# Optimization experiments

Measured on AMD Instinct MI355X. Metric: run time of the kernel, lower is better.

## Reference

```python
import jax, jax.numpy as jnp
import numpy as np

# Dimensions
B, T_ENC, T_DEC = 64, 128, 64          # batch, encoder frames, max_video_length
DH, DV, CHUNK = 1024, 2048, 8          # dim_hidden, dim_video, ON-LSTM chunk size
NCH = DV // CHUNK                      # number of chunks (256)
G = 4 * DV + 2 * NCH                   # gate width of ON-LSTM cell


def setup_inputs() -> dict:
    key = jax.random.key(0)
    ks = jax.random.split(key, 6)
    s = lambda n: 1.0 / np.sqrt(n)
    return {
        "encoder_outputs": jax.random.normal(ks[0], (B, T_ENC, DH), jnp.float32),
        "encoder_hidden": jnp.zeros((1, B, DH), jnp.float32),  # unused by forward
        # Attention_update params: score over concat(enc_feat, query)
        "W_att1": (jax.random.normal(ks[1], (DH + DV, DH), jnp.float32) * s(DH + DV)),
        "b_att1": jnp.zeros((DH,), jnp.float32),
        "w_att2": (jax.random.normal(ks[2], (DH,), jnp.float32) * s(DH)),
        # ON-LSTM cell params (single layer: input DH -> hidden DV)
        "W_ih": (jax.random.normal(ks[3], (DH, G), jnp.float32) * s(DH)),
        "b_ih": jnp.zeros((G,), jnp.float32),
        "W_hh": (jax.random.normal(ks[4], (DV, G), jnp.float32) * s(DV)),
        "b_hh": jnp.zeros((G,), jnp.float32),
    }


def cumsoftmax(x):
    return jnp.cumsum(jax.nn.softmax(x, axis=-1), axis=-1)


def _decode(encoder_outputs, W_att1, b_att1, w_att2, W_ih, b_ih, W_hh, b_hh):
    b = encoder_outputs.shape[0]
    t_enc = encoder_outputs.shape[1]
    h0 = jnp.zeros((b, DV), encoder_outputs.dtype)
    c0 = jnp.zeros((b, NCH, CHUNK), encoder_outputs.dtype)

    def step(carry, _):
        h, c = carry
        # --- attention: additive score over encoder outputs, query = hidden ---
        q = jnp.broadcast_to(h[:, None, :], (b, t_enc, DV))
        feat = jnp.concatenate([encoder_outputs, q], axis=-1)        # (B,T,DH+DV)
        e = jnp.tanh(feat @ W_att1 + b_att1) @ w_att2                # (B,T)
        alpha = jax.nn.softmax(e, axis=-1)
        context = jnp.einsum("bt,btd->bd", alpha, encoder_outputs)  # (B,DH)
        # --- ON-LSTM cell ---
        gates = context @ W_ih + b_ih + h @ W_hh + b_hh              # (B,G)
        cingate = 1.0 - cumsoftmax(gates[:, :NCH])                   # master input gate
        cforgetgate = cumsoftmax(gates[:, NCH:2 * NCH])              # master forget gate
        r = gates[:, 2 * NCH:].reshape(b, 4 * NCH, CHUNK)
        o = jax.nn.sigmoid(r[:, :NCH])
        g = jnp.tanh(r[:, NCH:2 * NCH])
        i = jax.nn.sigmoid(r[:, 2 * NCH:3 * NCH])
        f = jax.nn.sigmoid(r[:, 3 * NCH:])
        cin = cingate[:, :, None]
        cfg = cforgetgate[:, :, None]
        overlap = cfg * cin
        fgate = f * overlap + (cfg - overlap)
        igate = i * overlap + (cin - overlap)
        cy = fgate * c + igate * g                                   # (B,NCH,CHUNK)
        hy = (o * jnp.tanh(cy)).reshape(b, DV)
        return (hy, cy), hy

    (_, _), outs = jax.lax.scan(step, (h0, c0), None, length=T_DEC)
    return jnp.transpose(outs, (1, 0, 2))  # (B, T_DEC, DV)


def reference(encoder_outputs, encoder_hidden, W_att1, b_att1, w_att2, W_ih, b_ih, W_hh, b_hh):
    return _decode(encoder_outputs, W_att1, b_att1, w_att2, W_ih, b_ih, W_hh, b_hh)
```

## Files before the change

### kernel.cpp

```cpp
#include <hip/hip_runtime.h>
#include <math.h>

#define BB   64
#define TENC 128
#define TDEC 64
#define DHH  1024
#define DVV  2048
#define NCHN 256
#define GG   8704
#define KTOT 3072

typedef unsigned short u16;
typedef __bf16 bf16x8 __attribute__((ext_vector_type(8)));
typedef float  f32x4  __attribute__((ext_vector_type(4)));

__device__ __forceinline__ u16 f2bf(float f) {
    unsigned u = __float_as_uint(f);
    unsigned r = (u + 0x7fffu + ((u >> 16) & 1u)) >> 16;
    return (u16)r;
}
__device__ __forceinline__ float bf2f(u16 s) { return __uint_as_float(((unsigned)s) << 16); }
__device__ __forceinline__ float tanh_fast(float x) {
    float xc = fminf(fmaxf(x, -15.f), 15.f);
    float t = __expf(2.f * xc);
    return 1.f - 2.f * __builtin_amdgcn_rcpf(t + 1.f);
}
__device__ __forceinline__ float sigmoid_fast(float x) {
    float xc = fminf(fmaxf(x, -30.f), 30.f);
    return __builtin_amdgcn_rcpf(1.f + __expf(-xc));
}


__global__ __launch_bounds__(256) void k_init2(float* __restrict__ c,
                                               u16* __restrict__ xh,
                                               u16* __restrict__ xl) {
    int i = blockIdx.x * 256 + threadIdx.x;
    xh[i] = 0; xl[i] = 0;
    if (i < BB * DVV) c[i] = 0.f;
}

template <bool LO>
__global__ __launch_bounds__(256) void k_cvt(const float* __restrict__ S1,
                                             const float* __restrict__ S2,
                                             int K1, int N, int K,
                                             u16* __restrict__ Dh,
                                             u16* __restrict__ Dl) {
    __shared__ float t[64][65];
    int n0 = blockIdx.x * 64, k0 = blockIdx.y * 64;
    int tid = threadIdx.x;
    int cn = tid & 63, r4 = tid >> 6;
#pragma unroll
    for (int p = 0; p < 16; ++p) {
        int kk = p * 4 + r4;
        int kg = k0 + kk;
        const float* src = (kg < K1) ? S1 + (size_t)kg * N : S2 + (size_t)(kg - K1) * N;
        t[kk][cn] = src[n0 + cn];
    }
    __syncthreads();
    int ck = tid & 63, n4 = tid >> 6;
#pragma unroll
    for (int p = 0; p < 16; ++p) {
        int nn = p * 4 + n4;
        float w = t[ck][nn];
        u16 hi = f2bf(w);
        size_t o = (size_t)(n0 + nn) * K + k0 + ck;
        Dh[o] = hi;
        if (LO) Dl[o] = f2bf(w - bf2f(hi));
    }
}

__global__ __launch_bounds__(256) void k_cvt_rm(const float* __restrict__ src,
                                                u16* __restrict__ dh,
                                                u16* __restrict__ dl, int n) {
    for (int i = blockIdx.x * 256 + threadIdx.x; i < n; i += gridDim.x * 256) {
        float w = src[i];
        u16 hi = f2bf(w);
        dh[i] = hi;
        dl[i] = f2bf(w - bf2f(hi));
    }
}

__global__ __launch_bounds__(256) void k_mmaP(const u16* __restrict__ ench,
                                              const u16* __restrict__ encl,
                                              const u16* __restrict__ W1h,
                                              const u16* __restrict__ W1l,
                                              const float* __restrict__ b1,
                                              float* __restrict__ P) {
    int n0 = blockIdx.x * 64, m0 = blockIdx.y * 64;
    int wv = threadIdx.x >> 6, l = threadIdx.x & 63;
    int lr = l & 15, lk = (l >> 4) * 8;
    int n = n0 + wv * 16 + lr;
    const u16* wph = W1h + (size_t)n * DHH + lk;
    const u16* wpl = W1l + (size_t)n * DHH + lk;
    const u16* aph = ench + (size_t)(m0 + lr) * DHH + lk;
    const u16* apl = encl + (size_t)(m0 + lr) * DHH + lk;
    f32x4 z = {0.f, 0.f, 0.f, 0.f};
    f32x4 acc[4] = {z, z, z, z};
    for (int k = 0; k < DHH; k += 32) {
        bf16x8 bh = *(const bf16x8*)(wph + k);
        bf16x8 bl = *(const bf16x8*)(wpl + k);
#pragma unroll
        for (int mf = 0; mf < 4; ++mf) {
            size_t ao = (size_t)mf * 16 * DHH + k;
            bf16x8 ah = *(const bf16x8*)(aph + ao);
            bf16x8 al = *(const bf16x8*)(apl + ao);
            acc[mf] = __builtin_amdgcn_mfma_f32_16x16x32_bf16(ah, bh, acc[mf], 0, 0, 0);
            acc[mf] = __builtin_amdgcn_mfma_f32_16x16x32_bf16(ah, bl, acc[mf], 0, 0, 0);
            acc[mf] = __builtin_amdgcn_mfma_f32_16x16x32_bf16(al, bh, acc[mf], 0, 0, 0);
        }
    }
    float bias = b1[n];
#pragma unroll
    for (int mf = 0; mf < 4; ++mf)
#pragma unroll
        for (int r = 0; r < 4; ++r) {
            int m = m0 + mf * 16 + (l >> 4) * 4 + r;
            P[(size_t)m * DHH + n] = acc[mf][r] + bias;
        }
}

__global__ __launch_bounds__(256) void k_P(const float* __restrict__ enc,
                                           const float* __restrict__ W1,
                                           const float* __restrict__ b1,
                                           float* __restrict__ P) {
    __shared__ float As[32][68];
    __shared__ float Bs[32][68];
    int j0 = blockIdx.x * 64;
    int m0 = blockIdx.y * 64;
    int tid = threadIdx.x;
    int jg = tid & 15, bg = tid >> 4;
    float acc[4][4] = {};
    for (int k0 = 0; k0 < DHH; k0 += 32) {
#pragma unroll
        for (int p = 0; p < 8; ++p) {
            int r = p * 8 + (tid >> 5);
            int kk = tid & 31;
            As[kk][r] = enc[(size_t)(m0 + r) * DHH + k0 + kk];
        }
#pragma unroll
        for (int p = 0; p < 8; ++p) {
            int kk = p * 4 + (tid >> 6);
            int jl = tid & 63;
            Bs[kk][jl] = W1[(size_t)(k0 + kk) * DHH + j0 + jl];
        }
        __syncthreads();
#pragma unroll
        for (int kk = 0; kk < 32; ++kk) {
            float4 a = *(const float4*)&As[kk][bg * 4];
            float4 b = *(const float4*)&Bs[kk][jg * 4];
            float av[4] = {a.x, a.y, a.z, a.w};
            float bv[4] = {b.x, b.y, b.z, b.w};
#pragma unroll
            for (int i = 0; i < 4; ++i)
#pragma unroll
                for (int j = 0; j < 4; ++j) acc[i][j] += av[i] * bv[j];
        }
        __syncthreads();
    }
    float4 bb = *(const float4*)&b1[j0 + jg * 4];
    float bia[4] = {bb.x, bb.y, bb.z, bb.w};
#pragma unroll
    for (int i = 0; i < 4; ++i) {
        int r = m0 + bg * 4 + i;
        float4 v = make_float4(acc[i][0] + bia[0], acc[i][1] + bia[1],
                               acc[i][2] + bia[2], acc[i][3] + bia[3]);
        *(float4*)&P[(size_t)r * DHH + j0 + jg * 4] = v;
    }
}


__global__ __launch_bounds__(512) void k_mma1(const u16* __restrict__ xh,
                                              const u16* __restrict__ Wta,
                                              float* __restrict__ hWp) {
    __shared__ float red[64 * 68];
    int n0 = blockIdx.x * 64;
    int kseg = blockIdx.y;
    int tid = threadIdx.x;
    int wv = tid >> 6, l = tid & 63;
    int wn = wv & 3, kh = wv >> 2;
    int lr = l & 15, lk = (l >> 4) * 8;
    int n = n0 + wn * 16 + lr;
    const u16* wp = Wta + (size_t)n * 2048 + lk;
    const u16* ap = xh + (size_t)lr * KTOT + 1024 + lk;
    f32x4 z = {0.f, 0.f, 0.f, 0.f};
    f32x4 acc[4] = {z, z, z, z};
    int kbeg = kseg * 256 + kh * 128;
    for (int k = kbeg; k < kbeg + 128; k += 32) {
        bf16x8 bfrag = *(const bf16x8*)(wp + k);
#pragma unroll
        for (int mf = 0; mf < 4; ++mf) {
            bf16x8 a = *(const bf16x8*)(ap + (size_t)mf * 16 * KTOT + k);
            acc[mf] = __builtin_amdgcn_mfma_f32_16x16x32_bf16(a, bfrag, acc[mf], 0, 0, 0);
        }
    }
    int moff = (l >> 4) * 4;
    if (kh == 0) {
#pragma unroll
        for (int mf = 0; mf < 4; ++mf)
#pragma unroll
            for (int r = 0; r < 4; ++r)
                red[(mf * 16 + moff + r) * 68 + wn * 16 + lr] = acc[mf][r];
    }
    __syncthreads();
    if (kh == 1) {
        float* dst = hWp + (size_t)kseg * 64 * DHH;
#pragma unroll
        for (int mf = 0; mf < 4; ++mf)
#pragma unroll
            for (int r = 0; r < 4; ++r) {
                int m = mf * 16 + moff + r;
                dst[(size_t)m * DHH + n] = acc[mf][r] + red[m * 68 + wn * 16 + lr];
            }
    }
}

template <int SEG>
__global__ __launch_bounds__(512) void k_mma3(const u16* __restrict__ xh,
                                              const u16* __restrict__ xl,
                                              const u16* __restrict__ Wh,
                                              const u16* __restrict__ Wl,
                                              float* __restrict__ part) {
    __shared__ float red[64 * 68];
    int n0 = blockIdx.x * 64;
    int kseg = blockIdx.y;
    int tid = threadIdx.x;
    int wv = tid >> 6, l = tid & 63;
    int wn = wv & 3, kh = wv >> 2;
    int lr = l & 15, lk = (l >> 4) * 8;
    int n = n0 + wn * 16 + lr;
    const u16* wph = Wh + (size_t)n * KTOT + lk;
    const u16* wpl = Wl + (size_t)n * KTOT + lk;
    const u16* aph = xh + (size_t)lr * KTOT + lk;
    const u16* apl = xl + (size_t)lr * KTOT + lk;
    f32x4 z = {0.f, 0.f, 0.f, 0.f};
    f32x4 acc[4] = {z, z, z, z};
    const int KSEG = KTOT / SEG;
    const int KH = KSEG / 2;
    int kbeg = kseg * KSEG + kh * KH;
    for (int k = kbeg; k < kbeg + KH; k += 32) {
        bf16x8 bh = *(const bf16x8*)(wph + k);
        bf16x8 bl = *(const bf16x8*)(wpl + k);
#pragma unroll
        for (int mf = 0; mf < 4; ++mf) {
            size_t ao = (size_t)mf * 16 * KTOT + k;
            bf16x8 ah = *(const bf16x8*)(aph + ao);
            bf16x8 al = *(const bf16x8*)(apl + ao);
            acc[mf] = __builtin_amdgcn_mfma_f32_16x16x32_bf16(ah, bh, acc[mf], 0, 0, 0);
            acc[mf] = __builtin_amdgcn_mfma_f32_16x16x32_bf16(ah, bl, acc[mf], 0, 0, 0);
            acc[mf] = __builtin_amdgcn_mfma_f32_16x16x32_bf16(al, bh, acc[mf], 0, 0, 0);
        }
    }
    int moff = (l >> 4) * 4;
    if (kh == 0) {
#pragma unroll
        for (int mf = 0; mf < 4; ++mf)
#pragma unroll
            for (int r = 0; r < 4; ++r)
                red[(mf * 16 + moff + r) * 68 + wn * 16 + lr] = acc[mf][r];
    }
    __syncthreads();
    if (kh == 1) {
        float* dst = part + (size_t)kseg * 64 * GG;
#pragma unroll
        for (int mf = 0; mf < 4; ++mf)
#pragma unroll
            for (int r = 0; r < 4; ++r) {
                int m = mf * 16 + moff + r;
                dst[(size_t)m * GG + n] = acc[mf][r] + red[m * 68 + wn * 16 + lr];
            }
    }
}

__global__ __launch_bounds__(256) void k_e(const float* __restrict__ P,
                                           const float* __restrict__ hWp,
                                           const float* __restrict__ w2,
                                           float* __restrict__ e) {
    int b = blockIdx.x, tg = blockIdx.y;
    __shared__ float hw[DHH];
    __shared__ float w2s[DHH];
    int tid = threadIdx.x;
    {
        float4 s = {0.f, 0.f, 0.f, 0.f};
#pragma unroll
        for (int ks = 0; ks < 8; ++ks) {
            float4 v = *(const float4*)&hWp[(size_t)(ks * 64 + b) * DHH + tid * 4];
            s.x += v.x; s.y += v.y; s.z += v.z; s.w += v.w;
        }
        *(float4*)&hw[tid * 4] = s;
        *(float4*)&w2s[tid * 4] = *(const float4*)&w2[tid * 4];
    }
    __syncthreads();
    int wave = tid >> 6, lane = tid & 63;
    const float* Pb = P + (size_t)b * TENC * DHH;
    for (int tt = 0; tt < 8; ++tt) {
        int t = tg * 32 + wave * 8 + tt;
        const float* Pr = Pb + (size_t)t * DHH;
        float s = 0.f;
#pragma unroll
        for (int i = 0; i < 16; ++i) {
            int d = i * 64 + lane;
            s += tanh_fast(Pr[d] + hw[d]) * w2s[d];
        }
#pragma unroll
        for (int off = 32; off > 0; off >>= 1) s += __shfl_down(s, off);
        if (lane == 0) e[b * TENC + t] = s;
    }
}

__global__ __launch_bounds__(256) void k_sc2(const float* __restrict__ e,
                                             const float* __restrict__ enc,
                                             u16* __restrict__ xh,
                                             u16* __restrict__ xl) {
    int b = blockIdx.x, dq = blockIdx.y;
    __shared__ float al[TENC];
    __shared__ float red[256];
    __shared__ float4 pr[4][64];
    int tid = threadIdx.x;
    float v = (tid < TENC) ? e[b * TENC + tid] : -3.0e38f;
    red[tid] = v;
    __syncthreads();
    for (int s = 128; s > 0; s >>= 1) {
        if (tid < s) red[tid] = fmaxf(red[tid], red[tid + s]);
        __syncthreads();
    }
    float mx = red[0];
    __syncthreads();
    float ex = (tid < TENC) ? __expf(v - mx) : 0.f;
    red[tid] = ex;
    __syncthreads();
    for (int s = 128; s > 0; s >>= 1) {
        if (tid < s) red[tid] += red[tid + s];
        __syncthreads();
    }
    float inv = 1.f / red[0];
    if (tid < TENC) al[tid] = ex * inv;
    __syncthreads();
    int w = tid >> 6, l = tid & 63;
    int dbase = dq * 256 + l * 4;
    const float* ep = enc + ((size_t)b * TENC + w * 32) * DHH + dbase;
    float4 acc = {0.f, 0.f, 0.f, 0.f};
#pragma unroll 8
    for (int tt = 0; tt < 32; ++tt) {
        float a = al[w * 32 + tt];
        float4 vv = *(const float4*)(ep + (size_t)tt * DHH);
        acc.x += a * vv.x; acc.y += a * vv.y; acc.z += a * vv.z; acc.w += a * vv.w;
    }
    pr[w][l] = acc;
    __syncthreads();
    if (tid < 64) {
        float4 a0 = pr[0][tid], a1 = pr[1][tid], a2 = pr[2][tid], a3 = pr[3][tid];
        float r0 = a0.x + a1.x + a2.x + a3.x;
        float r1 = a0.y + a1.y + a2.y + a3.y;
        float r2 = a0.z + a1.z + a2.z + a3.z;
        float r3 = a0.w + a1.w + a2.w + a3.w;
        size_t o = (size_t)b * KTOT + dq * 256 + tid * 4;
        u16 h0 = f2bf(r0), h1 = f2bf(r1), h2 = f2bf(r2), h3 = f2bf(r3);
        ushort4 hv = {h0, h1, h2, h3};
        ushort4 lv = {f2bf(r0 - bf2f(h0)), f2bf(r1 - bf2f(h1)),
                      f2bf(r2 - bf2f(h2)), f2bf(r3 - bf2f(h3))};
        *(ushort4*)&xh[o] = hv;
        *(ushort4*)&xl[o] = lv;
    }
}

__global__ __launch_bounds__(256) void k_pw2(const float* __restrict__ part, int nseg,
                                             const float* __restrict__ bih,
                                             const float* __restrict__ bhh,
                                             u16* __restrict__ xh,
                                             u16* __restrict__ xl,
                                             float* __restrict__ c,
                                             float* __restrict__ out, int t) {
    int b = blockIdx.x;
    __shared__ float g[GG];
    __shared__ float cs1[NCHN], cs2[NCHN], t1[NCHN], t2[NCHN];
    int tid = threadIdx.x;
    for (int p = 0; p < 34; ++p) {
        int j = p * 256 + tid;
        float s = bih[j] + bhh[j];
        for (int ks = 0; ks < nseg; ++ks) s += part[(size_t)(ks * 64 + b) * GG + j];
        g[j] = s;
    }
    __syncthreads();
    float x1 = g[tid], x2 = g[NCHN + tid];
    t1[tid] = x1; t2[tid] = x2;
    __syncthreads();
    for (int s = 128; s > 0; s >>= 1) {
        if (tid < s) { t1[tid] = fmaxf(t1[tid], t1[tid + s]); t2[tid] = fmaxf(t2[tid], t2[tid + s]); }
        __syncthreads();
    }
    float m1 = t1[0], m2 = t2[0];
    __syncthreads();
    float e1 = __expf(x1 - m1), e2 = __expf(x2 - m2);
    t1[tid] = e1; t2[tid] = e2;
    __syncthreads();
    for (int s = 128; s > 0; s >>= 1) {
        if (tid < s) { t1[tid] += t1[tid + s]; t2[tid] += t2[tid + s]; }
        __syncthreads();
    }
    float inv1 = 1.f / t1[0], inv2 = 1.f / t2[0];
    __syncthreads();
    cs1[tid] = e1; cs2[tid] = e2;
    __syncthreads();
    for (int off = 1; off < NCHN; off <<= 1) {
        float a1 = (tid >= off) ? cs1[tid - off] : 0.f;
        float a2 = (tid >= off) ? cs2[tid - off] : 0.f;
        __syncthreads();
        cs1[tid] += a1; cs2[tid] += a2;
        __syncthreads();
    }
    float* cb = c + (size_t)b * DVV;
    float* ob = out + ((size_t)b * TDEC + t) * DVV;
    u16* xhb = xh + (size_t)b * KTOT + 1024;
    u16* xlb = xl + (size_t)b * KTOT + 1024;
    for (int p = 0; p < 8; ++p) {
        int idx = p * 256 + tid;
        int ch = idx >> 3;
        float cin = 1.f - cs1[ch] * inv1;
        float cfg = cs2[ch] * inv2;
        float ov = cfg * cin;
        float oo = sigmoid_fast(g[512 + idx]);
        float gg = tanh_fast(g[2560 + idx]);
        float ii = sigmoid_fast(g[4608 + idx]);
        float ff = sigmoid_fast(g[6656 + idx]);
        float fg = ff * ov + (cfg - ov);
        float ig = ii * ov + (cin - ov);
        float cy = fg * cb[idx] + ig * gg;
        cb[idx] = cy;
        float hy = oo * tanh_fast(cy);
        ob[idx] = hy;
        u16 hh = f2bf(hy);
        xhb[idx] = hh;
        xlb[idx] = f2bf(hy - bf2f(hh));
    }
}


extern "C" void kernel_launch(void* const* d_in, const int* in_sizes, int n_in,
                              void* d_out, int out_size, void* d_ws, size_t ws_size,
                              hipStream_t stream) {
    const float* enc    = (const float*)d_in[0];
    const float* W_att1 = (const float*)d_in[2];
    const float* b_att1 = (const float*)d_in[3];
    const float* w_att2 = (const float*)d_in[4];
    const float* W_ih   = (const float*)d_in[5];
    const float* b_ih   = (const float*)d_in[6];
    const float* W_hh   = (const float*)d_in[7];
    const float* b_hh   = (const float*)d_in[8];
    float* out = (float*)d_out;
    float* ws  = (float*)d_ws;
    const float* Wh_att = W_att1 + 1024 * 1024;

    if (ws_size >= 182976512ull) {
        float* P   = ws;
        float* c   = P + 8388608;
        u16* Wth   = (u16*)(c + 131072);
        u16* Wtl   = Wth + 26738688;
        u16* Wta   = Wtl + 26738688;
        u16* region = Wta + 2097152;
        u16* ench = region;
        u16* encl = ench + 8388608;
        u16* W1h  = encl + 8388608;
        u16* W1l  = W1h + 1048576;
        float* gp   = (float*)region;
        float* hWp  = gp + 2228224;
        float* ebuf = hWp + 524288;
        u16* xh     = (u16*)(ebuf + 8192);
        u16* xl     = xh + 196608;

        k_cvt<true><<<dim3(136, 48), 256, 0, stream>>>(W_ih, W_hh, 1024, GG, KTOT, Wth, Wtl);
        k_cvt<false><<<dim3(16, 32), 256, 0, stream>>>(Wh_att, Wh_att, 2048, DHH, 2048, Wta, Wta);
        k_cvt<true><<<dim3(16, 16), 256, 0, stream>>>(W_att1, W_att1, 2048, DHH, DHH, W1h, W1l);
        k_cvt_rm<<<4096, 256, 0, stream>>>(enc, ench, encl, 8388608);
        k_mmaP<<<dim3(16, 128), 256, 0, stream>>>(ench, encl, W1h, W1l, b_att1, P);
        k_init2<<<768, 256, 0, stream>>>(c, xh, xl);

        for (int t = 0; t < TDEC; ++t) {
            k_mma1<<<dim3(16, 8), 512, 0, stream>>>(xh, Wta, hWp);
            k_e<<<dim3(BB, 4), 256, 0, stream>>>(P, hWp, w_att2, ebuf);
            k_sc2<<<dim3(BB, 4), 256, 0, stream>>>(ebuf, enc, xh, xl);
            k_mma3<4><<<dim3(136, 4), 512, 0, stream>>>(xh, xl, Wth, Wtl, gp);
            k_pw2<<<BB, 256, 0, stream>>>(gp, 4, b_ih, b_hh, xh, xl, c, out, t);
        }
    } else if (ws_size >= 152600576ull) {
        float* P    = ws;
        float* hWp  = P + 8388608;
        float* ebuf = hWp + 524288;
        float* gp   = ebuf + 8192;
        float* c    = gp + 1114112;
        u16* xh  = (u16*)(c + 131072);
        u16* xl  = xh + 196608;
        u16* Wth = xl + 196608;
        u16* Wtl = Wth + 26738688;
        u16* Wta = Wtl + 26738688;

        k_cvt<true><<<dim3(136, 48), 256, 0, stream>>>(W_ih, W_hh, 1024, GG, KTOT, Wth, Wtl);
        k_cvt<false><<<dim3(16, 32), 256, 0, stream>>>(Wh_att, Wh_att, 2048, DHH, 2048, Wta, Wta);
        k_P<<<dim3(16, 128), 256, 0, stream>>>(enc, W_att1, b_att1, P);
        k_init2<<<768, 256, 0, stream>>>(c, xh, xl);

        for (int t = 0; t < TDEC; ++t) {
            k_mma1<<<dim3(16, 8), 512, 0, stream>>>(xh, Wta, hWp);
            k_e<<<dim3(BB, 4), 256, 0, stream>>>(P, hWp, w_att2, ebuf);
            k_sc2<<<dim3(BB, 4), 256, 0, stream>>>(ebuf, enc, xh, xl);
            k_mma3<2><<<dim3(136, 2), 512, 0, stream>>>(xh, xl, Wth, Wtl, gp);
            k_pw2<<<BB, 256, 0, stream>>>(gp, 2, b_ih, b_hh, xh, xl, c, out, t);
        }
    }
}
```

Baseline: 10.14 ms.

## Fuse decode loop into one persistent cooperative kernel with grid barriers

```diff
diff --git a/kernel.cpp b/kernel.cpp
--- a/kernel.cpp
+++ b/kernel.cpp
@@ -30,13 +30,29 @@
     return __builtin_amdgcn_rcpf(1.f + __expf(-xc));
 }
 
-
-__global__ __launch_bounds__(256) void k_init2(float* __restrict__ c,
-                                               u16* __restrict__ xh,
-                                               u16* __restrict__ xl) {
+__device__ __forceinline__ void gbar(int* cnt, int* gen) {
+    __syncthreads();
+    __threadfence();
+    if (threadIdx.x == 0) {
+        int g = atomicAdd(gen, 0);
+        if (atomicAdd(cnt, 1) == (int)gridDim.x - 1) {
+            atomicExch(cnt, 0);
+            __threadfence();
+            atomicAdd(gen, 1);
+        } else {
+            while (atomicAdd(gen, 0) == g) __builtin_amdgcn_s_sleep(2);
+        }
+    }
+    __syncthreads();
+    __threadfence();
+}
+
+
+__global__ __launch_bounds__(256) void k_init2(float* c, u16* xh, u16* xl, int* bar) {
     int i = blockIdx.x * 256 + threadIdx.x;
     xh[i] = 0; xl[i] = 0;
     if (i < BB * DVV) c[i] = 0.f;
+    if (i < 4) bar[i] = 0;
 }
 
 template <bool LO>
@@ -69,60 +85,10 @@
     }
 }
 
-__global__ __launch_bounds__(256) void k_cvt_rm(const float* __restrict__ src,
-                                                u16* __restrict__ dh,
-                                                u16* __restrict__ dl, int n) {
-    for (int i = blockIdx.x * 256 + threadIdx.x; i < n; i += gridDim.x * 256) {
-        float w = src[i];
-        u16 hi = f2bf(w);
-        dh[i] = hi;
-        dl[i] = f2bf(w - bf2f(hi));
-    }
-}
-
-__global__ __launch_bounds__(256) void k_mmaP(const u16* __restrict__ ench,
-                                              const u16* __restrict__ encl,
-                                              const u16* __restrict__ W1h,
-                                              const u16* __restrict__ W1l,
-                                              const float* __restrict__ b1,
-                                              float* __restrict__ P) {
-    int n0 = blockIdx.x * 64, m0 = blockIdx.y * 64;
-    int wv = threadIdx.x >> 6, l = threadIdx.x & 63;
-    int lr = l & 15, lk = (l >> 4) * 8;
-    int n = n0 + wv * 16 + lr;
-    const u16* wph = W1h + (size_t)n * DHH + lk;
-    const u16* wpl = W1l + (size_t)n * DHH + lk;
-    const u16* aph = ench + (size_t)(m0 + lr) * DHH + lk;
-    const u16* apl = encl + (size_t)(m0 + lr) * DHH + lk;
-    f32x4 z = {0.f, 0.f, 0.f, 0.f};
-    f32x4 acc[4] = {z, z, z, z};
-    for (int k = 0; k < DHH; k += 32) {
-        bf16x8 bh = *(const bf16x8*)(wph + k);
-        bf16x8 bl = *(const bf16x8*)(wpl + k);
-#pragma unroll
-        for (int mf = 0; mf < 4; ++mf) {
-            size_t ao = (size_t)mf * 16 * DHH + k;
-            bf16x8 ah = *(const bf16x8*)(aph + ao);
-            bf16x8 al = *(const bf16x8*)(apl + ao);
-            acc[mf] = __builtin_amdgcn_mfma_f32_16x16x32_bf16(ah, bh, acc[mf], 0, 0, 0);
-            acc[mf] = __builtin_amdgcn_mfma_f32_16x16x32_bf16(ah, bl, acc[mf], 0, 0, 0);
-            acc[mf] = __builtin_amdgcn_mfma_f32_16x16x32_bf16(al, bh, acc[mf], 0, 0, 0);
-        }
-    }
-    float bias = b1[n];
-#pragma unroll
-    for (int mf = 0; mf < 4; ++mf)
-#pragma unroll
-        for (int r = 0; r < 4; ++r) {
-            int m = m0 + mf * 16 + (l >> 4) * 4 + r;
-            P[(size_t)m * DHH + n] = acc[mf][r] + bias;
-        }
-}
-
-__global__ __launch_bounds__(256) void k_P(const float* __restrict__ enc,
-                                           const float* __restrict__ W1,
-                                           const float* __restrict__ b1,
-                                           float* __restrict__ P) {
+__global__ __launch_bounds__(256) void k_Pb(const float* __restrict__ enc,
+                                            const float* __restrict__ W1,
+                                            const float* __restrict__ b1,
+                                            u16* __restrict__ Pb) {
     __shared__ float As[32][68];
     __shared__ float Bs[32][68];
     int j0 = blockIdx.x * 64;
@@ -162,9 +128,273 @@
 #pragma unroll
     for (int i = 0; i < 4; ++i) {
         int r = m0 + bg * 4 + i;
-        float4 v = make_float4(acc[i][0] + bia[0], acc[i][1] + bia[1],
-                               acc[i][2] + bia[2], acc[i][3] + bia[3]);
-        *(float4*)&P[(size_t)r * DHH + j0 + jg * 4] = v;
+        ushort4 sv;
+        sv.x = f2bf(acc[i][0] + bia[0]);
+        sv.y = f2bf(acc[i][1] + bia[1]);
+        sv.z = f2bf(acc[i][2] + bia[2]);
+        sv.w = f2bf(acc[i][3] + bia[3]);
+        *(ushort4*)&Pb[(size_t)r * DHH + j0 + jg * 4] = sv;
+    }
+}
+
+
+__global__ __launch_bounds__(512) void k_decode(
+        const u16* Pbf, float* hWp, float* ebuf, float* gp, float* c,
+        u16* xh, u16* xl,
+        const u16* __restrict__ Wth, const u16* __restrict__ Wtl,
+        const u16* __restrict__ Wta,
+        const float* __restrict__ enc, const float* __restrict__ w2,
+        const float* __restrict__ bih, const float* __restrict__ bhh,
+        float* out, int* bar) {
+    __shared__ float smem[9728];
+    int* cnt = bar;
+    int* gen = bar + 1;
+    int blk = blockIdx.x, tid = threadIdx.x;
+    int wv = tid >> 6, l = tid & 63;
+    int lr = l & 15, lk4 = l >> 4;
+    f32x4 z = {0.f, 0.f, 0.f, 0.f};
+
+    for (int t = 0; t < TDEC; ++t) {
+        {
+            int nt = blk & 15, kseg = blk >> 4;
+            int wn = wv & 3, kh = wv >> 2;
+            int n = nt * 64 + wn * 16 + lr;
+            int kb = kseg * 128 + kh * 64;
+            const u16* wp = Wta + (size_t)n * 2048 + kb + lk4 * 8;
+            const u16* ap = xh + (size_t)lr * KTOT + 1024 + kb + lk4 * 8;
+            f32x4 acc[4] = {z, z, z, z};
+#pragma unroll
+            for (int kk = 0; kk < 64; kk += 32) {
+                bf16x8 bfrag = *(const bf16x8*)(wp + kk);
+#pragma unroll
+                for (int mf = 0; mf < 4; ++mf) {
+                    bf16x8 a = *(const bf16x8*)(ap + (size_t)mf * 16 * KTOT + kk);
+                    acc[mf] = __builtin_amdgcn_mfma_f32_16x16x32_bf16(a, bfrag, acc[mf], 0, 0, 0);
+                }
+            }
+            float* red = smem;
+            if (kh == 0) {
+#pragma unroll
+                for (int mf = 0; mf < 4; ++mf)
+#pragma unroll
+                    for (int r = 0; r < 4; ++r)
+                        red[(mf * 16 + lk4 * 4 + r) * 68 + wn * 16 + lr] = acc[mf][r];
+            }
+            __syncthreads();
+            if (kh == 1) {
+#pragma unroll
+                for (int mf = 0; mf < 4; ++mf)
+#pragma unroll
+                    for (int r = 0; r < 4; ++r) {
+                        int m = mf * 16 + lk4 * 4 + r;
+                        hWp[(size_t)(kseg * 64 + m) * DHH + n] =
+                            acc[mf][r] + red[m * 68 + wn * 16 + lr];
+                    }
+            }
+        }
+        gbar(cnt, gen);
+
+        {
+            int b = blk >> 2, tg = blk & 3;
+            float* hw = smem;
+            float* w2s = smem + 1024;
+#pragma unroll
+            for (int p = 0; p < 2; ++p) {
+                int d = p * 512 + tid;
+                float s = 0.f;
+#pragma unroll
+                for (int ks = 0; ks < 16; ++ks) s += hWp[(size_t)(ks * 64 + b) * DHH + d];
+                hw[d] = s;
+                w2s[d] = w2[d];
+            }
+            __syncthreads();
+            const u16* Pb = Pbf + (size_t)b * TENC * DHH;
+#pragma unroll
+            for (int i = 0; i < 4; ++i) {
+                int tt = tg * 32 + wv * 4 + i;
+                const u16* Pr = Pb + (size_t)tt * DHH;
+                float s = 0.f;
+#pragma unroll
+                for (int q = 0; q < 16; ++q) {
+                    int d = q * 64 + l;
+                    s += tanh_fast(bf2f(Pr[d]) + hw[d]) * w2s[d];
+                }
+#pragma unroll
+                for (int off = 32; off > 0; off >>= 1) s += __shfl_down(s, off);
+                if (l == 0) ebuf[b * TENC + tt] = s;
+            }
+        }
+        gbar(cnt, gen);
+
+        {
+            int b = blk >> 2, dq = blk & 3;
+            float* al = smem;
+            float* red = smem + 128;
+            float4* pr = (float4*)(smem + 640);
+            float v = (tid < TENC) ? ebuf[b * TENC + tid] : -3.0e38f;
+            red[tid] = v;
+            __syncthreads();
+            for (int s = 256; s > 0; s >>= 1) {
+                if (tid < s) red[tid] = fmaxf(red[tid], red[tid + s]);
+                __syncthreads();
+            }
+            float mx = red[0];
+            __syncthreads();
+            float ex = (tid < TENC) ? __expf(v - mx) : 0.f;
+            red[tid] = ex;
+            __syncthreads();
+            for (int s = 256; s > 0; s >>= 1) {
+                if (tid < s) red[tid] += red[tid + s];
+                __syncthreads();
+            }
+            float inv = 1.f / red[0];
+            if (tid < TENC) al[tid] = ex * inv;
+            __syncthreads();
+            const float* ep = enc + ((size_t)b * TENC + wv * 16) * DHH + dq * 256 + l * 4;
+            float4 acc = {0.f, 0.f, 0.f, 0.f};
+#pragma unroll 4
+            for (int j = 0; j < 16; ++j) {
+                float a = al[wv * 16 + j];
+                float4 vv = *(const float4*)(ep + (size_t)j * DHH);
+                acc.x += a * vv.x; acc.y += a * vv.y; acc.z += a * vv.z; acc.w += a * vv.w;
+            }
+            pr[wv * 64 + l] = acc;
+            __syncthreads();
+            if (tid < 64) {
+                float r0 = 0.f, r1 = 0.f, r2 = 0.f, r3 = 0.f;
+#pragma unroll
+                for (int k = 0; k < 8; ++k) {
+                    float4 a = pr[k * 64 + tid];
+                    r0 += a.x; r1 += a.y; r2 += a.z; r3 += a.w;
+                }
+                size_t o = (size_t)b * KTOT + dq * 256 + tid * 4;
+                u16 h0 = f2bf(r0), h1 = f2bf(r1), h2 = f2bf(r2), h3 = f2bf(r3);
+                ushort4 hv = {h0, h1, h2, h3};
+                ushort4 lv = {f2bf(r0 - bf2f(h0)), f2bf(r1 - bf2f(h1)),
+                              f2bf(r2 - bf2f(h2)), f2bf(r3 - bf2f(h3))};
+                *(ushort4*)&xh[o] = hv;
+                *(ushort4*)&xl[o] = lv;
+            }
+        }
+        gbar(cnt, gen);
+
+        {
+            int gw = blk * 8 + wv;
+            for (int task = gw; task < 2176; task += 2048) {
+                int nt = task >> 3;
+                int kq = task & 7;
+                int kb = kq * 384;
+                int n0 = nt * 32 + lr;
+                const u16* wph0 = Wth + (size_t)n0 * KTOT + kb + lk4 * 8;
+                const u16* wpl0 = Wtl + (size_t)n0 * KTOT + kb + lk4 * 8;
+                const u16* wph1 = wph0 + (size_t)16 * KTOT;
+                const u16* wpl1 = wpl0 + (size_t)16 * KTOT;
+                const u16* aph = xh + (size_t)lr * KTOT + kb + lk4 * 8;
+                const u16* apl = xl + (size_t)lr * KTOT + kb + lk4 * 8;
+                f32x4 acc0[4] = {z, z, z, z};
+                f32x4 acc1[4] = {z, z, z, z};
+                for (int kk = 0; kk < 384; kk += 32) {
+                    bf16x8 bh0 = *(const bf16x8*)(wph0 + kk);
+                    bf16x8 bl0 = *(const bf16x8*)(wpl0 + kk);
+                    bf16x8 bh1 = *(const bf16x8*)(wph1 + kk);
+                    bf16x8 bl1 = *(const bf16x8*)(wpl1 + kk);
+#pragma unroll
+                    for (int mf = 0; mf < 4; ++mf) {
+                        size_t ao = (size_t)mf * 16 * KTOT + kk;
+                        bf16x8 ah = *(const bf16x8*)(aph + ao);
+                        bf16x8 al_ = *(const bf16x8*)(apl + ao);
+                        acc0[mf] = __builtin_amdgcn_mfma_f32_16x16x32_bf16(ah, bh0, acc0[mf], 0, 0, 0);
+                        acc0[mf] = __builtin_amdgcn_mfma_f32_16x16x32_bf16(ah, bl0, acc0[mf], 0, 0, 0);
+                        acc0[mf] = __builtin_amdgcn_mfma_f32_16x16x32_bf16(al_, bh0, acc0[mf], 0, 0, 0);
+                        acc1[mf] = __builtin_amdgcn_mfma_f32_16x16x32_bf16(ah, bh1, acc1[mf], 0, 0, 0);
+                        acc1[mf] = __builtin_amdgcn_mfma_f32_16x16x32_bf16(ah, bl1, acc1[mf], 0, 0, 0);
+                        acc1[mf] = __builtin_amdgcn_mfma_f32_16x16x32_bf16(al_, bh1, acc1[mf], 0, 0, 0);
+                    }
+                }
+                float* dst = gp + (size_t)kq * 64 * GG;
+#pragma unroll
+                for (int mf = 0; mf < 4; ++mf)
+#pragma unroll
+                    for (int r = 0; r < 4; ++r) {
+                        int m = mf * 16 + lk4 * 4 + r;
+                        dst[(size_t)m * GG + nt * 32 + lr] = acc0[mf][r];
+                        dst[(size_t)m * GG + nt * 32 + 16 + lr] = acc1[mf][r];
+                    }
+            }
+        }
+        gbar(cnt, gen);
+
+        if (blk < BB) {
+            int b = blk;
+            float* g = smem;
+            float* cs1 = smem + 8704;
+            float* cs2 = cs1 + 256;
+            float* r1 = cs2 + 256;
+            float* r2 = r1 + 256;
+#pragma unroll 2
+            for (int p = 0; p < 17; ++p) {
+                int j = p * 512 + tid;
+                float s = bih[j] + bhh[j];
+#pragma unroll
+                for (int ks = 0; ks < 8; ++ks) s += gp[(size_t)(ks * 64 + b) * GG + j];
+                g[j] = s;
+            }
+            __syncthreads();
+            float x1 = 0.f, x2 = 0.f;
+            if (tid < 256) { x1 = g[tid]; x2 = g[NCHN + tid]; r1[tid] = x1; r2[tid] = x2; }
+            __syncthreads();
+            for (int s = 128; s > 0; s >>= 1) {
+                if (tid < s) { r1[tid] = fmaxf(r1[tid], r1[tid + s]); r2[tid] = fmaxf(r2[tid], r2[tid + s]); }
+                __syncthreads();
+            }
+            float m1 = r1[0], m2 = r2[0];
+            __syncthreads();
+            float e1 = 0.f, e2 = 0.f;
+            if (tid < 256) {
+                e1 = __expf(x1 - m1); e2 = __expf(x2 - m2);
+                r1[tid] = e1; r2[tid] = e2; cs1[tid] = e1; cs2[tid] = e2;
+            }
+            __syncthreads();
+            for (int s = 128; s > 0; s >>= 1) {
+                if (tid < s) { r1[tid] += r1[tid + s]; r2[tid] += r2[tid + s]; }
+                __syncthreads();
+            }
+            float inv1 = 1.f / r1[0], inv2 = 1.f / r2[0];
+            __syncthreads();
+            for (int off = 1; off < NCHN; off <<= 1) {
+                float a1 = 0.f, a2 = 0.f;
+                if (tid < NCHN && tid >= off) { a1 = cs1[tid - off]; a2 = cs2[tid - off]; }
+                __syncthreads();
+                if (tid < NCHN) { cs1[tid] += a1; cs2[tid] += a2; }
+                __syncthreads();
+            }
+            float* cb = c + (size_t)b * DVV;
+            float* ob = out + ((size_t)b * TDEC + t) * DVV;
+            u16* xhb = xh + (size_t)b * KTOT + 1024;
+            u16* xlb = xl + (size_t)b * KTOT + 1024;
+#pragma unroll
+            for (int p = 0; p < 4; ++p) {
+                int idx = p * 512 + tid;
+                int ch = idx >> 3;
+                float cin = 1.f - cs1[ch] * inv1;
+                float cfg = cs2[ch] * inv2;
+                float ov = cfg * cin;
+                float oo = sigmoid_fast(g[512 + idx]);
+                float gg = tanh_fast(g[2560 + idx]);
+                float ii = sigmoid_fast(g[4608 + idx]);
+                float ff = sigmoid_fast(g[6656 + idx]);
+                float fg = ff * ov + (cfg - ov);
+                float ig = ii * ov + (cin - ov);
+                float cy = fg * cb[idx] + ig * gg;
+                cb[idx] = cy;
+                float hy = oo * tanh_fast(cy);
+                ob[idx] = hy;
+                u16 hh = f2bf(hy);
+                xhb[idx] = hh;
+                xlb[idx] = f2bf(hy - bf2f(hh));
+            }
+        }
+        gbar(cnt, gen);
     }
 }
 
@@ -211,6 +441,98 @@
                 int m = mf * 16 + moff + r;
                 dst[(size_t)m * DHH + n] = acc[mf][r] + red[m * 68 + wn * 16 + lr];
             }
+    }
+}
+
+__global__ __launch_bounds__(256) void k_e_bf(const u16* __restrict__ Pbf,
+                                              const float* __restrict__ hWp,
+                                              const float* __restrict__ w2,
+                                              float* __restrict__ e) {
+    int b = blockIdx.x, tg = blockIdx.y;
+    __shared__ float hw[DHH];
+    __shared__ float w2s[DHH];
+    int tid = threadIdx.x;
+    {
+        float4 s = {0.f, 0.f, 0.f, 0.f};
+#pragma unroll
+        for (int ks = 0; ks < 8; ++ks) {
+            float4 v = *(const float4*)&hWp[(size_t)(ks * 64 + b) * DHH + tid * 4];
+            s.x += v.x; s.y += v.y; s.z += v.z; s.w += v.w;
+        }
+        *(float4*)&hw[tid * 4] = s;
+        *(float4*)&w2s[tid * 4] = *(const float4*)&w2[tid * 4];
+    }
+    __syncthreads();
+    int wave = tid >> 6, lane = tid & 63;
+    const u16* Pb = Pbf + (size_t)b * TENC * DHH;
+    for (int tt = 0; tt < 8; ++tt) {
+        int t = tg * 32 + wave * 8 + tt;
+        const u16* Pr = Pb + (size_t)t * DHH;
+        float s = 0.f;
+#pragma unroll
+        for (int i = 0; i < 16; ++i) {
+            int d = i * 64 + lane;
+            s += tanh_fast(bf2f(Pr[d]) + hw[d]) * w2s[d];
+        }
+#pragma unroll
+        for (int off = 32; off > 0; off >>= 1) s += __shfl_down(s, off);
+        if (lane == 0) e[b * TENC + t] = s;
+    }
+}
+
+__global__ __launch_bounds__(256) void k_sc2(const float* __restrict__ e,
+                                             const float* __restrict__ enc,
+                                             u16* __restrict__ xh,
+                                             u16* __restrict__ xl) {
+    int b = blockIdx.x, dq = blockIdx.y;
+    __shared__ float al[TENC];
+    __shared__ float red[256];
+    __shared__ float4 pr[4][64];
+    int tid = threadIdx.x;
+    float v = (tid < TENC) ? e[b * TENC + tid] : -3.0e38f;
+    red[tid] = v;
+    __syncthreads();
+    for (int s = 128; s > 0; s >>= 1) {
+        if (tid < s) red[tid] = fmaxf(red[tid], red[tid + s]);
+        __syncthreads();
+    }
+    float mx = red[0];
+    __syncthreads();
+    float ex = (tid < TENC) ? __expf(v - mx) : 0.f;
+    red[tid] = ex;
+    __syncthreads();
+    for (int s = 128; s > 0; s >>= 1) {
+        if (tid < s) red[tid] += red[tid + s];
+        __syncthreads();
+    }
+    float inv = 1.f / red[0];
+    if (tid < TENC) al[tid] = ex * inv;
+    __syncthreads();
+    int w = tid >> 6, l = tid & 63;
+    int dbase = dq * 256 + l * 4;
+    const float* ep = enc + ((size_t)b * TENC + w * 32) * DHH + dbase;
+    float4 acc = {0.f, 0.f, 0.f, 0.f};
+#pragma unroll 8
+    for (int tt = 0; tt < 32; ++tt) {
+        float a = al[w * 32 + tt];
+        float4 vv = *(const float4*)(ep + (size_t)tt * DHH);
+        acc.x += a * vv.x; acc.y += a * vv.y; acc.z += a * vv.z; acc.w += a * vv.w;
+    }
+    pr[w][l] = acc;
+    __syncthreads();
+    if (tid < 64) {
+        float4 a0 = pr[0][tid], a1 = pr[1][tid], a2 = pr[2][tid], a3 = pr[3][tid];
+        float r0 = a0.x + a1.x + a2.x + a3.x;
+        float r1 = a0.y + a1.y + a2.y + a3.y;
+        float r2 = a0.z + a1.z + a2.z + a3.z;
+        float r3 = a0.w + a1.w + a2.w + a3.w;
+        size_t o = (size_t)b * KTOT + dq * 256 + tid * 4;
+        u16 h0 = f2bf(r0), h1 = f2bf(r1), h2 = f2bf(r2), h3 = f2bf(r3);
+        ushort4 hv = {h0, h1, h2, h3};
+        ushort4 lv = {f2bf(r0 - bf2f(h0)), f2bf(r1 - bf2f(h1)),
+                      f2bf(r2 - bf2f(h2)), f2bf(r3 - bf2f(h3))};
+        *(ushort4*)&xh[o] = hv;
+        *(ushort4*)&xl[o] = lv;
     }
 }
 
@@ -271,98 +593,6 @@
     }
 }
 
-__global__ __launch_bounds__(256) void k_e(const float* __restrict__ P,
-                                           const float* __restrict__ hWp,
-                                           const float* __restrict__ w2,
-                                           float* __restrict__ e) {
-    int b = blockIdx.x, tg = blockIdx.y;
-    __shared__ float hw[DHH];
-    __shared__ float w2s[DHH];
-    int tid = threadIdx.x;
-    {
-        float4 s = {0.f, 0.f, 0.f, 0.f};
-#pragma unroll
-        for (int ks = 0; ks < 8; ++ks) {
-            float4 v = *(const float4*)&hWp[(size_t)(ks * 64 + b) * DHH + tid * 4];
-            s.x += v.x; s.y += v.y; s.z += v.z; s.w += v.w;
-        }
-        *(float4*)&hw[tid * 4] = s;
-        *(float4*)&w2s[tid * 4] = *(const float4*)&w2[tid * 4];
-    }
-    __syncthreads();
-    int wave = tid >> 6, lane = tid & 63;
-    const float* Pb = P + (size_t)b * TENC * DHH;
-    for (int tt = 0; tt < 8; ++tt) {
-        int t = tg * 32 + wave * 8 + tt;
-        const float* Pr = Pb + (size_t)t * DHH;
-        float s = 0.f;
-#pragma unroll
-        for (int i = 0; i < 16; ++i) {
-            int d = i * 64 + lane;
-            s += tanh_fast(Pr[d] + hw[d]) * w2s[d];
-        }
-#pragma unroll
-        for (int off = 32; off > 0; off >>= 1) s += __shfl_down(s, off);
-        if (lane == 0) e[b * TENC + t] = s;
-    }
-}
-
-__global__ __launch_bounds__(256) void k_sc2(const float* __restrict__ e,
-                                             const float* __restrict__ enc,
-                                             u16* __restrict__ xh,
-                                             u16* __restrict__ xl) {
-    int b = blockIdx.x, dq = blockIdx.y;
-    __shared__ float al[TENC];
-    __shared__ float red[256];
-    __shared__ float4 pr[4][64];
-    int tid = threadIdx.x;
-    float v = (tid < TENC) ? e[b * TENC + tid] : -3.0e38f;
-    red[tid] = v;
-    __syncthreads();
-    for (int s = 128; s > 0; s >>= 1) {
-        if (tid < s) red[tid] = fmaxf(red[tid], red[tid + s]);
-        __syncthreads();
-    }
-    float mx = red[0];
-    __syncthreads();
-    float ex = (tid < TENC) ? __expf(v - mx) : 0.f;
-    red[tid] = ex;
-    __syncthreads();
-    for (int s = 128; s > 0; s >>= 1) {
-        if (tid < s) red[tid] += red[tid + s];
-        __syncthreads();
-    }
-    float inv = 1.f / red[0];
-    if (tid < TENC) al[tid] = ex * inv;
-    __syncthreads();
-    int w = tid >> 6, l = tid & 63;
-    int dbase = dq * 256 + l * 4;
-    const float* ep = enc + ((size_t)b * TENC + w * 32) * DHH + dbase;
-    float4 acc = {0.f, 0.f, 0.f, 0.f};
-#pragma unroll 8
-    for (int tt = 0; tt < 32; ++tt) {
-        float a = al[w * 32 + tt];
-        float4 vv = *(const float4*)(ep + (size_t)tt * DHH);
-        acc.x += a * vv.x; acc.y += a * vv.y; acc.z += a * vv.z; acc.w += a * vv.w;
-    }
-    pr[w][l] = acc;
-    __syncthreads();
-    if (tid < 64) {
-        float4 a0 = pr[0][tid], a1 = pr[1][tid], a2 = pr[2][tid], a3 = pr[3][tid];
-        float r0 = a0.x + a1.x + a2.x + a3.x;
-        float r1 = a0.y + a1.y + a2.y + a3.y;
-        float r2 = a0.z + a1.z + a2.z + a3.z;
-        float r3 = a0.w + a1.w + a2.w + a3.w;
-        size_t o = (size_t)b * KTOT + dq * 256 + tid * 4;
-        u16 h0 = f2bf(r0), h1 = f2bf(r1), h2 = f2bf(r2), h3 = f2bf(r3);
-        ushort4 hv = {h0, h1, h2, h3};
-        ushort4 lv = {f2bf(r0 - bf2f(h0)), f2bf(r1 - bf2f(h1)),
-                      f2bf(r2 - bf2f(h2)), f2bf(r3 - bf2f(h3))};
-        *(ushort4*)&xh[o] = hv;
-        *(ushort4*)&xl[o] = lv;
-    }
-}
-
 __global__ __launch_bounds__(256) void k_pw2(const float* __restrict__ part, int nseg,
                                              const float* __restrict__ bih,
                                              const float* __restrict__ bhh,
@@ -450,60 +680,38 @@
     float* ws  = (float*)d_ws;
     const float* Wh_att = W_att1 + 1024 * 1024;
 
-    if (ws_size >= 182976512ull) {
-        float* P   = ws;
-        float* c   = P + 8388608;
-        u16* Wth   = (u16*)(c + 131072);
-        u16* Wtl   = Wth + 26738688;
-        u16* Wta   = Wtl + 26738688;
-        u16* region = Wta + 2097152;
-        u16* ench = region;
-        u16* encl = ench + 8388608;
-        u16* W1h  = encl + 8388608;
-        u16* W1l  = W1h + 1048576;
-        float* gp   = (float*)region;
-        float* hWp  = gp + 2228224;
-        float* ebuf = hWp + 524288;
-        u16* xh     = (u16*)(ebuf + 8192);
-        u16* xl     = xh + 196608;
-
-        k_cvt<true><<<dim3(136, 48), 256, 0, stream>>>(W_ih, W_hh, 1024, GG, KTOT, Wth, Wtl);
-        k_cvt<false><<<dim3(16, 32), 256, 0, stream>>>(Wh_att, Wh_att, 2048, DHH, 2048, Wta, Wta);
-        k_cvt<true><<<dim3(16, 16), 256, 0, stream>>>(W_att1, W_att1, 2048, DHH, DHH, W1h, W1l);
-        k_cvt_rm<<<4096, 256, 0, stream>>>(enc, ench, encl, 8388608);
-        k_mmaP<<<dim3(16, 128), 256, 0, stream>>>(ench, encl, W1h, W1l, b_att1, P);
-        k_init2<<<768, 256, 0, stream>>>(c, xh, xl);
-
+    float* hWp  = ws;
+    float* ebuf = hWp + 1048576;
+    float* gp   = ebuf + 8192;
+    float* c    = gp + 4456448;
+    int*   bar  = (int*)(c + 131072);
+    u16* Pbf = (u16*)(bar + 4);
+    u16* xh  = Pbf + 8388608;
+    u16* xl  = xh + 196608;
+    u16* Wth = xl + 196608;
+    u16* Wtl = Wth + 26738688;
+    u16* Wta = Wtl + 26738688;
+    if (ws_size < 151289872ull) return;
+
+    k_cvt<true><<<dim3(136, 48), 256, 0, stream>>>(W_ih, W_hh, 1024, GG, KTOT, Wth, Wtl);
+    k_cvt<false><<<dim3(16, 32), 256, 0, stream>>>(Wh_att, Wh_att, 2048, DHH, 2048, Wta, Wta);
+    k_Pb<<<dim3(16, 128), 256, 0, stream>>>(enc, W_att1, b_att1, Pbf);
+    k_init2<<<768, 256, 0, stream>>>(c, xh, xl, bar);
+
+    void* args[] = {(void*)&Pbf, (void*)&hWp, (void*)&ebuf, (void*)&gp, (void*)&c,
+                    (void*)&xh, (void*)&xl, (void*)&Wth, (void*)&Wtl, (void*)&Wta,
+                    (void*)&enc, (void*)&w_att2, (void*)&b_ih, (void*)&b_hh,
+                    (void*)&out, (void*)&bar};
+    hipError_t err = hipLaunchCooperativeKernel((const void*)k_decode,
+                                                dim3(256), dim3(512), args, 0, stream);
+    if (err != hipSuccess) {
+        (void)hipGetLastError();
         for (int t = 0; t < TDEC; ++t) {
             k_mma1<<<dim3(16, 8), 512, 0, stream>>>(xh, Wta, hWp);
-            k_e<<<dim3(BB, 4), 256, 0, stream>>>(P, hWp, w_att2, ebuf);
+            k_e_bf<<<dim3(BB, 4), 256, 0, stream>>>(Pbf, hWp, w_att2, ebuf);
             k_sc2<<<dim3(BB, 4), 256, 0, stream>>>(ebuf, enc, xh, xl);
             k_mma3<4><<<dim3(136, 4), 512, 0, stream>>>(xh, xl, Wth, Wtl, gp);
             k_pw2<<<BB, 256, 0, stream>>>(gp, 4, b_ih, b_hh, xh, xl, c, out, t);
         }
-    } else if (ws_size >= 152600576ull) {
-        float* P    = ws;
-        float* hWp  = P + 8388608;
-        float* ebuf = hWp + 524288;
-        float* gp   = ebuf + 8192;
-        float* c    = gp + 1114112;
-        u16* xh  = (u16*)(c + 131072);
-        u16* xl  = xh + 196608;
-        u16* Wth = xl + 196608;
-        u16* Wtl = Wth + 26738688;
-        u16* Wta = Wtl + 26738688;
-
-        k_cvt<true><<<dim3(136, 48), 256, 0, stream>>>(W_ih, W_hh, 1024, GG, KTOT, Wth, Wtl);
-        k_cvt<false><<<dim3(16, 32), 256, 0, stream>>>(Wh_att, Wh_att, 2048, DHH, 2048, Wta, Wta);
-        k_P<<<dim3(16, 128), 256, 0, stream>>>(enc, W_att1, b_att1, P);
-        k_init2<<<768, 256, 0, stream>>>(c, xh, xl);
-
-        for (int t = 0; t < TDEC; ++t) {
-            k_mma1<<<dim3(16, 8), 512, 0, stream>>>(xh, Wta, hWp);
-            k_e<<<dim3(BB, 4), 256, 0, stream>>>(P, hWp, w_att2, ebuf);
-            k_sc2<<<dim3(BB, 4), 256, 0, stream>>>(ebuf, enc, xh, xl);
-            k_mma3<2><<<dim3(136, 2), 512, 0, stream>>>(xh, xl, Wth, Wtl, gp);
-            k_pw2<<<BB, 256, 0, stream>>>(gp, 2, b_ih, b_hh, xh, xl, c, out, t);
-        }
-    }
-}
+    }
+}
```

Result: slower. 38.24 ms (+277.2%).
